# Performance work log

Hardware: AMD Instinct MI355X
Metric: run time of the kernel (lower is better)

Reference implementation:

```python
import jax, jax.numpy as jnp
import numpy as np

D_MODEL = 1024
NHEAD = 16
HEAD_DIM = D_MODEL // NHEAD
D_FF = 4096
LN_EPS = 1e-5


def _layernorm(x, gamma, beta):
    mu = jnp.mean(x, axis=-1, keepdims=True)
    var = jnp.mean(jnp.square(x - mu), axis=-1, keepdims=True)
    return (x - mu) * jax.lax.rsqrt(var + LN_EPS) * gamma + beta


def setup_inputs() -> dict:
    key = jax.random.key(0)
    ks = jax.random.split(key, 16)
    s = 1.0 / np.sqrt(D_MODEL)
    sf = 1.0 / np.sqrt(D_FF)
    inp = {
        "src": jax.random.normal(ks[0], (2, 2048, D_MODEL), dtype=jnp.float32),
        # projection weights stored [in, out]
        "Wq": jax.random.uniform(ks[1], (D_MODEL, D_MODEL), minval=-s, maxval=s),
        "bq": jax.random.uniform(ks[2], (D_MODEL,), minval=-s, maxval=s),
        "Wk": jax.random.uniform(ks[3], (D_MODEL, D_MODEL), minval=-s, maxval=s),
        "bk": jax.random.uniform(ks[4], (D_MODEL,), minval=-s, maxval=s),
        "Wv": jax.random.uniform(ks[5], (D_MODEL, D_MODEL), minval=-s, maxval=s),
        "bv": jax.random.uniform(ks[6], (D_MODEL,), minval=-s, maxval=s),
        "Wo": jax.random.uniform(ks[7], (D_MODEL, D_MODEL), minval=-s, maxval=s),
        "bo": jax.random.uniform(ks[8], (D_MODEL,), minval=-s, maxval=s),
        "W1": jax.random.uniform(ks[9], (D_MODEL, D_FF), minval=-s, maxval=s),
        "b1": jax.random.uniform(ks[10], (D_FF,), minval=-s, maxval=s),
        "W2": jax.random.uniform(ks[11], (D_FF, D_MODEL), minval=-sf, maxval=sf),
        "b2": jax.random.uniform(ks[12], (D_MODEL,), minval=-sf, maxval=sf),
        "gamma1": jnp.ones((D_MODEL,), jnp.float32),
        "beta1": jnp.zeros((D_MODEL,), jnp.float32),
        "gamma2": jnp.ones((D_MODEL,), jnp.float32),
        "beta2": jnp.zeros((D_MODEL,), jnp.float32),
    }
    return inp


def reference(src, Wq, bq, Wk, bk, Wv, bv, Wo, bo, W1, b1, W2, b2,
              gamma1, beta1, gamma2, beta2):
    B, L, D = src.shape
    H, Hd = NHEAD, HEAD_DIM
    # QKV projections -> [B, H, L, Hd]
    def split_heads(x):
        return x.reshape(B, L, H, Hd).transpose(0, 2, 1, 3)
    Q = split_heads(src @ Wq + bq)
    K = split_heads(src @ Wk + bk)
    V = split_heads(src @ Wv + bv)
    # attention (dropout is eval-mode identity)
    scores = jnp.einsum("bhqd,bhkd->bhqk", Q, K) / np.sqrt(Hd)
    probs = jax.nn.softmax(scores, axis=-1)
    attn = jnp.einsum("bhqk,bhkd->bhqd", probs, V)
    attn = attn.transpose(0, 2, 1, 3).reshape(B, L, D)
    attn = attn @ Wo + bo
    x = _layernorm(src + attn, gamma1, beta1)
    ff = jax.nn.gelu(x @ W1 + b1, approximate=False) @ W2 + b2
    return _layernorm(x + ff, gamma2, beta2)
```

## Files before the change

kernel.cpp:

```cpp
#include <hip/hip_runtime.h>
#include <cstdint>
#include <cstddef>

using short8 = short __attribute__((ext_vector_type(8)));
using f32x4  = float __attribute__((ext_vector_type(4)));

__device__ __forceinline__ unsigned short f2bf(float f) {
  unsigned int u = __float_as_uint(f);
  u += 0x7fffu + ((u >> 16) & 1u);
  return (unsigned short)(u >> 16);
}
__device__ __forceinline__ unsigned short f2bf_rhu(float f) {
  return (unsigned short)((__float_as_uint(f) + 0x8000u) >> 16);
}
__device__ __forceinline__ float bf2f(unsigned short s) {
  return __uint_as_float(((unsigned int)s) << 16);
}
__device__ __forceinline__ void async16(const void* g, void* l) {
  __builtin_amdgcn_global_load_lds(
      (const __attribute__((address_space(1))) unsigned int*)g,
      (__attribute__((address_space(3))) unsigned int*)l, 16, 0, 0);
}

#define D_MODEL 1024
#define NHEAD   16
#define HEADD   64
#define SEQL    2048
#define NTOK    4096
#define QSCALE  0.18033688011112042f

__global__ __launch_bounds__(256) void cvt_f32_bf16(const float* __restrict__ in,
                                                    unsigned short* __restrict__ out,
                                                    int n4) {
  int i = blockIdx.x * 256 + threadIdx.x;
  if (i >= n4) return;
  float4 v = ((const float4*)in)[i];
  union { unsigned long long u; unsigned short us[4]; } pk;
  pk.us[0] = f2bf(v.x); pk.us[1] = f2bf(v.y); pk.us[2] = f2bf(v.z); pk.us[3] = f2bf(v.w);
  ((unsigned long long*)out)[i] = pk.u;
}

struct TransTab {
  const float* src[6];
  unsigned short* dst[6];
  int R[6], C[6], start[6], shift[6];
};

__global__ __launch_bounds__(256) void transpose_all(TransTab tt) {
  int id = blockIdx.x, m = 0;
#pragma unroll
  for (int i = 1; i < 6; ++i) if (id >= tt.start[i]) m = i;
  const int local = id - tt.start[m];
  const int R = tt.R[m], C = tt.C[m];
  const int bc = (local & ((1 << tt.shift[m]) - 1)) * 32;
  const int br = (local >> tt.shift[m]) * 32;
  const float* in = tt.src[m];
  unsigned short* out = tt.dst[m];
  __shared__ float tile[32][33];
  const int tx = threadIdx.x & 31, ty = threadIdx.x >> 5;
#pragma unroll
  for (int i = 0; i < 32; i += 8)
    tile[ty + i][tx] = in[(size_t)(br + ty + i) * C + bc + tx];
  __syncthreads();
#pragma unroll
  for (int i = 0; i < 32; i += 8)
    out[(size_t)(bc + ty + i) * R + br + tx] = f2bf(tile[tx][ty + i]);
}

template <int MODE>
__global__ __launch_bounds__(256)
void gemm_bt(const unsigned short* __restrict__ A, const unsigned short* __restrict__ B,
             int M, int N, int K, int Kstride,
             const float* __restrict__ bias0, const float* __restrict__ bias1,
             const float* __restrict__ bias2,
             float* __restrict__ outF, unsigned short* __restrict__ outB,
             unsigned short* __restrict__ outQ, unsigned short* __restrict__ outK,
             unsigned short* __restrict__ outVT) {
  __shared__ __align__(16) short sA[128 * 32];
  __shared__ __align__(16) short sB[128 * 32];
  const int tid = threadIdx.x, wave = tid >> 6, lane = tid & 63;
  const int quad = lane >> 4, l16 = lane & 15;
  const int bm = blockIdx.y * 128, bn = blockIdx.x * 128;
  const int koff = blockIdx.z * K;
  const int wr = (wave >> 1) * 64, wc = (wave & 1) * 64;
  const f32x4 zero4 = {0.f, 0.f, 0.f, 0.f};
  f32x4 acc[4][4];
#pragma unroll
  for (int i = 0; i < 4; ++i)
#pragma unroll
    for (int j = 0; j < 4; ++j) acc[i][j] = zero4;

  for (int kt = 0; kt < K; kt += 32) {
    __syncthreads();
#pragma unroll
    for (int j = 0; j < 2; ++j) {
      int c = (wave * 2 + j) * 64 + lane;
      int row = c >> 2, cp = c & 3;
      int gk = koff + kt + ((cp ^ (row & 3)) * 8);
      async16(A + (size_t)(bm + row) * Kstride + gk, &sA[(wave * 2 + j) * 512]);
      async16(B + (size_t)(bn + row) * Kstride + gk, &sB[(wave * 2 + j) * 512]);
    }
    __syncthreads();
    short8 af[4], bfr[4];
#pragma unroll
    for (int i = 0; i < 4; ++i) {
      int ra = wr + i * 16 + l16;
      af[i] = *(const short8*)&sA[ra * 32 + ((quad ^ (l16 & 3)) * 8)];
      int rb = wc + i * 16 + l16;
      bfr[i] = *(const short8*)&sB[rb * 32 + ((quad ^ (l16 & 3)) * 8)];
    }
#pragma unroll
    for (int mi = 0; mi < 4; ++mi)
#pragma unroll
      for (int ni = 0; ni < 4; ++ni)
        acc[mi][ni] = __builtin_amdgcn_mfma_f32_16x16x32_bf16(af[mi], bfr[ni], acc[mi][ni], 0, 0, 0);
  }

#pragma unroll
  for (int mi = 0; mi < 4; ++mi)
#pragma unroll
    for (int ni = 0; ni < 4; ++ni) {
      const int col = bn + wc + ni * 16 + l16;
      const int row0 = bm + wr + mi * 16 + quad * 4;
      if constexpr (MODE == 0) {
        const int b_ = row0 >> 11, l_ = row0 & 2047;
        if (col < 1024) {
          const int hh = col >> 6, dd = col & 63;
          const size_t o = (((size_t)(b_ * NHEAD + hh)) * SEQL + l_) * HEADD + dd;
#pragma unroll
          for (int r = 0; r < 4; ++r)
            outQ[o + (size_t)r * HEADD] = f2bf((acc[mi][ni][r] + bias0[col]) * QSCALE);
        } else if (col < 2048) {
          const int n2 = col - 1024, hh = n2 >> 6, dd = n2 & 63;
          const size_t o = (((size_t)(b_ * NHEAD + hh)) * SEQL + l_) * HEADD + dd;
#pragma unroll
          for (int r = 0; r < 4; ++r)
            outK[o + (size_t)r * HEADD] = f2bf(acc[mi][ni][r] + bias1[n2]);
        } else {
          const int n2 = col - 2048, hh = n2 >> 6, dd = n2 & 63;
          union { unsigned long long u; unsigned short us[4]; } pk;
#pragma unroll
          for (int r = 0; r < 4; ++r) pk.us[r] = f2bf(acc[mi][ni][r] + bias2[n2]);
          *(unsigned long long*)&outVT[(((size_t)(b_ * NHEAD + hh)) * HEADD + dd) * SEQL + l_] = pk.u;
        }
      } else if constexpr (MODE == 1) {
        float* o = outF + (size_t)blockIdx.z * M * N + (size_t)row0 * N + col;
#pragma unroll
        for (int r = 0; r < 4; ++r) o[(size_t)r * N] = acc[mi][ni][r];
      } else {
#pragma unroll
        for (int r = 0; r < 4; ++r) {
          float x = acc[mi][ni][r] + bias0[col];
          float gl = 0.5f * x * (1.0f + erff(x * 0.70710678118654752f));
          outB[(size_t)(row0 + r) * N + col] = f2bf(gl);
        }
      }
    }
}

__global__ __launch_bounds__(256)
void flash_attn(const unsigned short* __restrict__ Qb, const unsigned short* __restrict__ Kb,
                const unsigned short* __restrict__ VTb, unsigned short* __restrict__ attnA) {
  __shared__ __align__(16) short sK[128 * 64];
  __shared__ __align__(16) short sV[64 * 128];
  __shared__ __align__(16) short sP[128 * 72];
  const int tid = threadIdx.x, wave = tid >> 6, lane = tid & 63;
  const int quad = lane >> 4, l16 = lane & 15;
  const int bh = blockIdx.y;
  const int q0 = blockIdx.x * 128;
  const size_t baseQK = (size_t)bh * SEQL * HEADD;
  const size_t baseV  = (size_t)bh * HEADD * SEQL;

#pragma unroll
  for (int j = 0; j < 4; ++j) {
    int c = (wave * 4 + j) * 64 + lane;
    int row = c >> 3, cp = c & 7;
    int gk = (cp ^ (row & 7)) * 8;
    async16(Qb + baseQK + (size_t)(q0 + row) * HEADD + gk, &sK[(wave * 4 + j) * 512]);
  }
  __syncthreads();
  short8 qf[2][2];
#pragma unroll
  for (int mi = 0; mi < 2; ++mi)
#pragma unroll
    for (int kk = 0; kk < 2; ++kk) {
      int m = wave * 32 + mi * 16 + l16;
      qf[mi][kk] = *(const short8*)&sK[m * 64 + (((kk * 4 + quad) ^ (m & 7)) * 8)];
    }

  const f32x4 zero4 = {0.f, 0.f, 0.f, 0.f};
  f32x4 o_acc[2][4];
  float lsum[2] = {0.f, 0.f};
#pragma unroll
  for (int mi = 0; mi < 2; ++mi)
#pragma unroll
    for (int ni = 0; ni < 4; ++ni) o_acc[mi][ni] = zero4;

  for (int t0 = 0; t0 < SEQL; t0 += 128) {
    __syncthreads();
#pragma unroll
    for (int j = 0; j < 4; ++j) {
      int c = (wave * 4 + j) * 64 + lane;
      { int row = c >> 3, cp = c & 7;
        int gk = (cp ^ (row & 7)) * 8;
        async16(Kb + baseQK + (size_t)(t0 + row) * HEADD + gk, &sK[(wave * 4 + j) * 512]); }
      { int d = c >> 4, cp = c & 15;
        int gl = (cp ^ (d & 15)) * 8;
        async16(VTb + baseV + (size_t)d * SEQL + t0 + gl, &sV[(wave * 4 + j) * 512]); }
    }
    __syncthreads();

#pragma unroll
    for (int h = 0; h < 2; ++h) {
      f32x4 st[4][2];
#pragma unroll
      for (int kt = 0; kt < 4; ++kt)
#pragma unroll
        for (int mi = 0; mi < 2; ++mi) st[kt][mi] = zero4;
#pragma unroll
      for (int kt = 0; kt < 4; ++kt) {
        int krow = (h * 4 + kt) * 16 + l16;
        short8 a0 = *(const short8*)&sK[krow * 64 + ((quad ^ (krow & 7)) * 8)];
        short8 a1 = *(const short8*)&sK[krow * 64 + (((4 + quad) ^ (krow & 7)) * 8)];
#pragma unroll
        for (int mi = 0; mi < 2; ++mi) {
          st[kt][mi] = __builtin_amdgcn_mfma_f32_16x16x32_bf16(a0, qf[mi][0], st[kt][mi], 0, 0, 0);
          st[kt][mi] = __builtin_amdgcn_mfma_f32_16x16x32_bf16(a1, qf[mi][1], st[kt][mi], 0, 0, 0);
        }
      }
#pragma unroll
      for (int kt = 0; kt < 4; ++kt)
#pragma unroll
        for (int mi = 0; mi < 2; ++mi) {
          float e0 = exp2f(st[kt][mi][0]);
          float e1 = exp2f(st[kt][mi][1]);
          float e2 = exp2f(st[kt][mi][2]);
          float e3 = exp2f(st[kt][mi][3]);
          lsum[mi] += (e0 + e1) + (e2 + e3);
          int q = wave * 32 + mi * 16 + l16;
          unsigned int* bp = (unsigned int*)&sP[q * 72 + kt * 16 + quad * 4];
          bp[0] = (unsigned)f2bf_rhu(e0) | ((unsigned)f2bf_rhu(e1) << 16);
          bp[1] = (unsigned)f2bf_rhu(e2) | ((unsigned)f2bf_rhu(e3) << 16);
        }
#pragma unroll
      for (int c = 0; c < 2; ++c) {
        short8 pf[2];
#pragma unroll
        for (int mi = 0; mi < 2; ++mi) {
          int q = wave * 32 + mi * 16 + l16;
          pf[mi] = *(const short8*)&sP[q * 72 + c * 32 + quad * 8];
        }
#pragma unroll
        for (int ni = 0; ni < 4; ++ni) {
          int vrow = ni * 16 + l16;
          short8 vf = *(const short8*)&sV[vrow * 128 + (((h * 8 + c * 4 + quad) ^ (vrow & 15)) * 8)];
#pragma unroll
          for (int mi = 0; mi < 2; ++mi)
            o_acc[mi][ni] = __builtin_amdgcn_mfma_f32_16x16x32_bf16(pf[mi], vf, o_acc[mi][ni], 0, 0, 0);
        }
      }
    }
  }

#pragma unroll
  for (int mi = 0; mi < 2; ++mi) {
    lsum[mi] += __shfl_xor(lsum[mi], 16, 64);
    lsum[mi] += __shfl_xor(lsum[mi], 32, 64);
  }
  const int b_ = bh >> 4, hh = bh & 15;
#pragma unroll
  for (int mi = 0; mi < 2; ++mi)
#pragma unroll
    for (int r = 0; r < 4; ++r) {
      float inv = 1.0f / __shfl(lsum[mi], quad * 4 + r, 64);
      int qrow = q0 + wave * 32 + mi * 16 + quad * 4 + r;
      size_t orow = ((size_t)(b_ * SEQL + qrow)) * D_MODEL + hh * HEADD;
#pragma unroll
      for (int ni = 0; ni < 4; ++ni)
        attnA[orow + ni * 16 + l16] = f2bf(o_acc[mi][ni][r] * inv);
    }
}

__device__ __forceinline__ void ln_core(float x0, float x1, float x2, float x3,
                                        const float* gamma, const float* beta,
                                        int tid, float& y0, float& y1, float& y2, float& y3) {
  float s = x0 + x1 + x2 + x3;
  float q = x0 * x0 + x1 * x1 + x2 * x2 + x3 * x3;
#pragma unroll
  for (int m = 1; m < 64; m <<= 1) {
    s += __shfl_xor(s, m, 64);
    q += __shfl_xor(q, m, 64);
  }
  __shared__ float red[8];
  const int wv = tid >> 6, ln = tid & 63;
  if (ln == 0) { red[wv] = s; red[4 + wv] = q; }
  __syncthreads();
  float S = red[0] + red[1] + red[2] + red[3];
  float Q2 = red[4] + red[5] + red[6] + red[7];
  float mu = S * (1.0f / 1024.0f);
  float var = Q2 * (1.0f / 1024.0f) - mu * mu;
  float rstd = rsqrtf(var + 1e-5f);
  float4 g = ((const float4*)gamma)[tid];
  float4 b = ((const float4*)beta)[tid];
  y0 = (x0 - mu) * rstd * g.x + b.x;
  y1 = (x1 - mu) * rstd * g.y + b.y;
  y2 = (x2 - mu) * rstd * g.z + b.z;
  y3 = (x3 - mu) * rstd * g.w + b.w;
}

__global__ __launch_bounds__(256)
void ln_combine1(const float* __restrict__ p, const float* __restrict__ src,
                 const float* __restrict__ bias, const float* __restrict__ gamma,
                 const float* __restrict__ beta, unsigned short* __restrict__ outB) {
  const int t = blockIdx.x, tid = threadIdx.x;
  const size_t MN = (size_t)NTOK * 1024, base = (size_t)t * 1024;
  float4 a = ((const float4*)(p + base))[tid];
  float4 b4 = ((const float4*)(p + MN + base))[tid];
  float4 s4 = ((const float4*)(src + base))[tid];
  float4 bi = ((const float4*)bias)[tid];
  float y0, y1, y2, y3;
  ln_core(a.x + b4.x + s4.x + bi.x, a.y + b4.y + s4.y + bi.y,
          a.z + b4.z + s4.z + bi.z, a.w + b4.w + s4.w + bi.w,
          gamma, beta, tid, y0, y1, y2, y3);
  union { unsigned long long u; unsigned short us[4]; } pk;
  pk.us[0] = f2bf(y0); pk.us[1] = f2bf(y1); pk.us[2] = f2bf(y2); pk.us[3] = f2bf(y3);
  ((unsigned long long*)(outB + base))[tid] = pk.u;
}

__global__ __launch_bounds__(256)
void ln_combine2(const float* __restrict__ p, const unsigned short* __restrict__ resB,
                 const float* __restrict__ bias, const float* __restrict__ gamma,
                 const float* __restrict__ beta, float* __restrict__ outF) {
  const int t = blockIdx.x, tid = threadIdx.x;
  const size_t MN = (size_t)NTOK * 1024, base = (size_t)t * 1024;
  float4 a = ((const float4*)(p + base))[tid];
  float4 b4 = ((const float4*)(p + MN + base))[tid];
  union { unsigned long long u; unsigned short us[4]; } r;
  r.u = ((const unsigned long long*)(resB + base))[tid];
  float4 bi = ((const float4*)bias)[tid];
  float y0, y1, y2, y3;
  ln_core(a.x + b4.x + bf2f(r.us[0]) + bi.x, a.y + b4.y + bf2f(r.us[1]) + bi.y,
          a.z + b4.z + bf2f(r.us[2]) + bi.z, a.w + b4.w + bf2f(r.us[3]) + bi.w,
          gamma, beta, tid, y0, y1, y2, y3);
  float4 o = {y0, y1, y2, y3};
  ((float4*)(outF + base))[tid] = o;
}

extern "C" void kernel_launch(void* const* d_in, const int* in_sizes, int n_in,
                              void* d_out, int out_size, void* d_ws, size_t ws_size,
                              hipStream_t stream) {
  const float* src    = (const float*)d_in[0];
  const float* Wq     = (const float*)d_in[1];
  const float* bq     = (const float*)d_in[2];
  const float* Wk     = (const float*)d_in[3];
  const float* bk     = (const float*)d_in[4];
  const float* Wv     = (const float*)d_in[5];
  const float* bv     = (const float*)d_in[6];
  const float* Wo     = (const float*)d_in[7];
  const float* bo     = (const float*)d_in[8];
  const float* W1     = (const float*)d_in[9];
  const float* b1     = (const float*)d_in[10];
  const float* W2     = (const float*)d_in[11];
  const float* b2     = (const float*)d_in[12];
  const float* gamma1 = (const float*)d_in[13];
  const float* beta1  = (const float*)d_in[14];
  const float* gamma2 = (const float*)d_in[15];
  const float* beta2  = (const float*)d_in[16];
  float* out = (float*)d_out;
  (void)in_sizes; (void)n_in; (void)out_size; (void)ws_size;

  char* p = (char*)d_ws;
  auto carve = [&](size_t n) { char* r = p; p += (n + 255) & ~(size_t)255; return r; };
  unsigned short* srcB  = (unsigned short*)carve((size_t)NTOK * 1024 * 2);
  unsigned short* WqkvT = (unsigned short*)carve((size_t)3072 * 1024 * 2);
  unsigned short* WoT   = (unsigned short*)carve((size_t)1024 * 1024 * 2);
  unsigned short* W1T   = (unsigned short*)carve((size_t)4096 * 1024 * 2);
  unsigned short* W2T   = (unsigned short*)carve((size_t)1024 * 4096 * 2);
  unsigned short* Qb    = (unsigned short*)carve((size_t)NTOK * 1024 * 2);
  unsigned short* Kb    = (unsigned short*)carve((size_t)NTOK * 1024 * 2);
  unsigned short* VTb   = (unsigned short*)carve((size_t)NTOK * 1024 * 2);
  carve((size_t)NTOK * 1024 * 2);
  unsigned short* xln   = (unsigned short*)carve((size_t)NTOK * 1024 * 2);
  unsigned short* hmid  = (unsigned short*)carve((size_t)NTOK * 4096 * 2);
  unsigned short* attnA = srcB;
  float* partial = (float*)Qb;

  cvt_f32_bf16<<<4096, 256, 0, stream>>>(src, srcB, NTOK * 1024 / 4);
  TransTab tt;
  tt.src[0] = Wq; tt.src[1] = Wk; tt.src[2] = Wv; tt.src[3] = Wo; tt.src[4] = W1; tt.src[5] = W2;
  tt.dst[0] = WqkvT; tt.dst[1] = WqkvT + 1024 * 1024; tt.dst[2] = WqkvT + 2 * 1024 * 1024;
  tt.dst[3] = WoT; tt.dst[4] = W1T; tt.dst[5] = W2T;
  for (int i = 0; i < 4; ++i) { tt.R[i] = 1024; tt.C[i] = 1024; tt.shift[i] = 5; }
  tt.R[4] = 1024; tt.C[4] = 4096; tt.shift[4] = 7;
  tt.R[5] = 4096; tt.C[5] = 1024; tt.shift[5] = 5;
  tt.start[0] = 0; tt.start[1] = 1024; tt.start[2] = 2048; tt.start[3] = 3072;
  tt.start[4] = 4096; tt.start[5] = 8192;
  transpose_all<<<12288, 256, 0, stream>>>(tt);

  gemm_bt<0><<<dim3(24, 32, 1), 256, 0, stream>>>(srcB, WqkvT, NTOK, 3072, 1024, 1024,
                                                  bq, bk, bv, nullptr, nullptr, Qb, Kb, VTb);
  flash_attn<<<dim3(16, 32), 256, 0, stream>>>(Qb, Kb, VTb, attnA);
  gemm_bt<1><<<dim3(8, 32, 2), 256, 0, stream>>>(attnA, WoT, NTOK, 1024, 512, 1024,
                                                 nullptr, nullptr, nullptr, partial,
                                                 nullptr, nullptr, nullptr, nullptr);
  ln_combine1<<<NTOK, 256, 0, stream>>>(partial, src, bo, gamma1, beta1, xln);
  gemm_bt<2><<<dim3(32, 32, 1), 256, 0, stream>>>(xln, W1T, NTOK, 4096, 1024, 1024,
                                                  b1, nullptr, nullptr, nullptr, hmid,
                                                  nullptr, nullptr, nullptr);
  gemm_bt<1><<<dim3(8, 32, 2), 256, 0, stream>>>(hmid, W2T, NTOK, 1024, 2048, 4096,
                                                 nullptr, nullptr, nullptr, partial,
                                                 nullptr, nullptr, nullptr, nullptr);
  ln_combine2<<<NTOK, 256, 0, stream>>>(partial, xln, b2, gamma2, beta2, out);
}
```

Before: 408.5 us.

## Deepen GEMM K tile, add split-K 4, approximate GELU, drop LDS for Q/K

Several independent changes land together. The GEMM now stages 64-wide K tiles with an 8-way XOR swizzle and declares 4 blocks per CU. Split-K for the output projections rises to 4 when workspace allows, and the LN kernels sum a variable number of partials. Exact erf GELU is replaced by a sigmoid-style exp2/rcp approximation. Flash attention reads Q and K fragments straight from global memory instead of staging them in LDS, and uses hardware exp2 plus perm-based bf16 packing. These aim to cut loop and sync overhead and to speed the epilogue math, at the cost of GELU accuracy and more uncoalesced K reads.

```diff
diff --git a/kernel.cpp b/kernel.cpp
--- a/kernel.cpp
+++ b/kernel.cpp
@@ -10,11 +10,13 @@
   u += 0x7fffu + ((u >> 16) & 1u);
   return (unsigned short)(u >> 16);
 }
-__device__ __forceinline__ unsigned short f2bf_rhu(float f) {
-  return (unsigned short)((__float_as_uint(f) + 0x8000u) >> 16);
-}
 __device__ __forceinline__ float bf2f(unsigned short s) {
   return __uint_as_float(((unsigned int)s) << 16);
+}
+__device__ __forceinline__ unsigned int pack_bf16_rhu(float lo, float hi) {
+  unsigned int a = __float_as_uint(lo) + 0x8000u;
+  unsigned int b = __float_as_uint(hi) + 0x8000u;
+  return __builtin_amdgcn_perm(b, a, 0x07060302u);
 }
 __device__ __forceinline__ void async16(const void* g, void* l) {
   __builtin_amdgcn_global_load_lds(
@@ -35,8 +37,9 @@
   int i = blockIdx.x * 256 + threadIdx.x;
   if (i >= n4) return;
   float4 v = ((const float4*)in)[i];
-  union { unsigned long long u; unsigned short us[4]; } pk;
-  pk.us[0] = f2bf(v.x); pk.us[1] = f2bf(v.y); pk.us[2] = f2bf(v.z); pk.us[3] = f2bf(v.w);
+  union { unsigned long long u; unsigned int ui[2]; } pk;
+  pk.ui[0] = pack_bf16_rhu(v.x, v.y);
+  pk.ui[1] = pack_bf16_rhu(v.z, v.w);
   ((unsigned long long*)out)[i] = pk.u;
 }
 
@@ -68,7 +71,7 @@
 }
 
 template <int MODE>
-__global__ __launch_bounds__(256)
+__global__ __launch_bounds__(256, 4)
 void gemm_bt(const unsigned short* __restrict__ A, const unsigned short* __restrict__ B,
              int M, int N, int K, int Kstride,
              const float* __restrict__ bias0, const float* __restrict__ bias1,
@@ -76,8 +79,8 @@
              float* __restrict__ outF, unsigned short* __restrict__ outB,
              unsigned short* __restrict__ outQ, unsigned short* __restrict__ outK,
              unsigned short* __restrict__ outVT) {
-  __shared__ __align__(16) short sA[128 * 32];
-  __shared__ __align__(16) short sB[128 * 32];
+  __shared__ __align__(16) short sA[128 * 64];
+  __shared__ __align__(16) short sB[128 * 64];
   const int tid = threadIdx.x, wave = tid >> 6, lane = tid & 63;
   const int quad = lane >> 4, l16 = lane & 15;
   const int bm = blockIdx.y * 128, bn = blockIdx.x * 128;
@@ -90,30 +93,33 @@
 #pragma unroll
     for (int j = 0; j < 4; ++j) acc[i][j] = zero4;
 
-  for (int kt = 0; kt < K; kt += 32) {
+  for (int kt = 0; kt < K; kt += 64) {
     __syncthreads();
 #pragma unroll
-    for (int j = 0; j < 2; ++j) {
-      int c = (wave * 2 + j) * 64 + lane;
-      int row = c >> 2, cp = c & 3;
-      int gk = koff + kt + ((cp ^ (row & 3)) * 8);
-      async16(A + (size_t)(bm + row) * Kstride + gk, &sA[(wave * 2 + j) * 512]);
-      async16(B + (size_t)(bn + row) * Kstride + gk, &sB[(wave * 2 + j) * 512]);
+    for (int j = 0; j < 4; ++j) {
+      int c = (wave * 4 + j) * 64 + lane;
+      int row = c >> 3, cp = c & 7;
+      int gk = koff + kt + ((cp ^ (row & 7)) * 8);
+      async16(A + (size_t)(bm + row) * Kstride + gk, &sA[(wave * 4 + j) * 512]);
+      async16(B + (size_t)(bn + row) * Kstride + gk, &sB[(wave * 4 + j) * 512]);
     }
     __syncthreads();
-    short8 af[4], bfr[4];
-#pragma unroll
-    for (int i = 0; i < 4; ++i) {
-      int ra = wr + i * 16 + l16;
-      af[i] = *(const short8*)&sA[ra * 32 + ((quad ^ (l16 & 3)) * 8)];
-      int rb = wc + i * 16 + l16;
-      bfr[i] = *(const short8*)&sB[rb * 32 + ((quad ^ (l16 & 3)) * 8)];
-    }
-#pragma unroll
-    for (int mi = 0; mi < 4; ++mi)
-#pragma unroll
-      for (int ni = 0; ni < 4; ++ni)
-        acc[mi][ni] = __builtin_amdgcn_mfma_f32_16x16x32_bf16(af[mi], bfr[ni], acc[mi][ni], 0, 0, 0);
+#pragma unroll
+    for (int kk = 0; kk < 2; ++kk) {
+      short8 af[4], bfr[4];
+#pragma unroll
+      for (int i = 0; i < 4; ++i) {
+        int ra = wr + i * 16 + l16;
+        af[i] = *(const short8*)&sA[ra * 64 + (((kk * 4 + quad) ^ (ra & 7)) * 8)];
+        int rb = wc + i * 16 + l16;
+        bfr[i] = *(const short8*)&sB[rb * 64 + (((kk * 4 + quad) ^ (rb & 7)) * 8)];
+      }
+#pragma unroll
+      for (int mi = 0; mi < 4; ++mi)
+#pragma unroll
+        for (int ni = 0; ni < 4; ++ni)
+          acc[mi][ni] = __builtin_amdgcn_mfma_f32_16x16x32_bf16(af[mi], bfr[ni], acc[mi][ni], 0, 0, 0);
+    }
   }
 
 #pragma unroll
@@ -151,7 +157,10 @@
 #pragma unroll
         for (int r = 0; r < 4; ++r) {
           float x = acc[mi][ni][r] + bias0[col];
-          float gl = 0.5f * x * (1.0f + erff(x * 0.70710678118654752f));
+          float x2 = x * x;
+          float z = x * fmaf(0.102944f, x2, 2.302208f);
+          float t = __builtin_amdgcn_exp2f(z);
+          float gl = x - x * __builtin_amdgcn_rcpf(t + 1.0f);
           outB[(size_t)(row0 + r) * N + col] = f2bf(gl);
         }
       }
@@ -161,7 +170,6 @@
 __global__ __launch_bounds__(256)
 void flash_attn(const unsigned short* __restrict__ Qb, const unsigned short* __restrict__ Kb,
                 const unsigned short* __restrict__ VTb, unsigned short* __restrict__ attnA) {
-  __shared__ __align__(16) short sK[128 * 64];
   __shared__ __align__(16) short sV[64 * 128];
   __shared__ __align__(16) short sP[128 * 72];
   const int tid = threadIdx.x, wave = tid >> 6, lane = tid & 63;
@@ -171,21 +179,13 @@
   const size_t baseQK = (size_t)bh * SEQL * HEADD;
   const size_t baseV  = (size_t)bh * HEADD * SEQL;
 
-#pragma unroll
-  for (int j = 0; j < 4; ++j) {
-    int c = (wave * 4 + j) * 64 + lane;
-    int row = c >> 3, cp = c & 7;
-    int gk = (cp ^ (row & 7)) * 8;
-    async16(Qb + baseQK + (size_t)(q0 + row) * HEADD + gk, &sK[(wave * 4 + j) * 512]);
-  }
-  __syncthreads();
   short8 qf[2][2];
 #pragma unroll
   for (int mi = 0; mi < 2; ++mi)
 #pragma unroll
     for (int kk = 0; kk < 2; ++kk) {
-      int m = wave * 32 + mi * 16 + l16;
-      qf[mi][kk] = *(const short8*)&sK[m * 64 + (((kk * 4 + quad) ^ (m & 7)) * 8)];
+      int q = q0 + wave * 32 + mi * 16 + l16;
+      qf[mi][kk] = *(const short8*)(Qb + baseQK + (size_t)q * HEADD + kk * 32 + quad * 8);
     }
 
   const f32x4 zero4 = {0.f, 0.f, 0.f, 0.f};
@@ -201,12 +201,9 @@
 #pragma unroll
     for (int j = 0; j < 4; ++j) {
       int c = (wave * 4 + j) * 64 + lane;
-      { int row = c >> 3, cp = c & 7;
-        int gk = (cp ^ (row & 7)) * 8;
-        async16(Kb + baseQK + (size_t)(t0 + row) * HEADD + gk, &sK[(wave * 4 + j) * 512]); }
-      { int d = c >> 4, cp = c & 15;
-        int gl = (cp ^ (d & 15)) * 8;
-        async16(VTb + baseV + (size_t)d * SEQL + t0 + gl, &sV[(wave * 4 + j) * 512]); }
+      int d = c >> 4, cp = c & 15;
+      int gl = (cp ^ (d & 15)) * 8;
+      async16(VTb + baseV + (size_t)d * SEQL + t0 + gl, &sV[(wave * 4 + j) * 512]);
     }
     __syncthreads();
 
@@ -219,9 +216,10 @@
         for (int mi = 0; mi < 2; ++mi) st[kt][mi] = zero4;
 #pragma unroll
       for (int kt = 0; kt < 4; ++kt) {
-        int krow = (h * 4 + kt) * 16 + l16;
-        short8 a0 = *(const short8*)&sK[krow * 64 + ((quad ^ (krow & 7)) * 8)];
-        short8 a1 = *(const short8*)&sK[krow * 64 + (((4 + quad) ^ (krow & 7)) * 8)];
+        const unsigned short* kp =
+            Kb + baseQK + (size_t)(t0 + h * 64 + kt * 16 + l16) * HEADD + quad * 8;
+        short8 a0 = *(const short8*)(kp);
+        short8 a1 = *(const short8*)(kp + 32);
 #pragma unroll
         for (int mi = 0; mi < 2; ++mi) {
           st[kt][mi] = __builtin_amdgcn_mfma_f32_16x16x32_bf16(a0, qf[mi][0], st[kt][mi], 0, 0, 0);
@@ -232,15 +230,16 @@
       for (int kt = 0; kt < 4; ++kt)
 #pragma unroll
         for (int mi = 0; mi < 2; ++mi) {
-          float e0 = exp2f(st[kt][mi][0]);
-          float e1 = exp2f(st[kt][mi][1]);
-          float e2 = exp2f(st[kt][mi][2]);
-          float e3 = exp2f(st[kt][mi][3]);
+          float e0 = __builtin_amdgcn_exp2f(st[kt][mi][0]);
+          float e1 = __builtin_amdgcn_exp2f(st[kt][mi][1]);
+          float e2 = __builtin_amdgcn_exp2f(st[kt][mi][2]);
+          float e3 = __builtin_amdgcn_exp2f(st[kt][mi][3]);
           lsum[mi] += (e0 + e1) + (e2 + e3);
           int q = wave * 32 + mi * 16 + l16;
-          unsigned int* bp = (unsigned int*)&sP[q * 72 + kt * 16 + quad * 4];
-          bp[0] = (unsigned)f2bf_rhu(e0) | ((unsigned)f2bf_rhu(e1) << 16);
-          bp[1] = (unsigned)f2bf_rhu(e2) | ((unsigned)f2bf_rhu(e3) << 16);
+          union { unsigned long long u; unsigned int ui[2]; } pk;
+          pk.ui[0] = pack_bf16_rhu(e0, e1);
+          pk.ui[1] = pack_bf16_rhu(e2, e3);
+          *(unsigned long long*)&sP[q * 72 + kt * 16 + quad * 4] = pk.u;
         }
 #pragma unroll
       for (int c = 0; c < 2; ++c) {
@@ -309,38 +308,45 @@
 }
 
 __global__ __launch_bounds__(256)
-void ln_combine1(const float* __restrict__ p, const float* __restrict__ src,
+void ln_combine1(const float* __restrict__ p, int nsplit, const float* __restrict__ src,
                  const float* __restrict__ bias, const float* __restrict__ gamma,
                  const float* __restrict__ beta, unsigned short* __restrict__ outB) {
   const int t = blockIdx.x, tid = threadIdx.x;
   const size_t MN = (size_t)NTOK * 1024, base = (size_t)t * 1024;
   float4 a = ((const float4*)(p + base))[tid];
-  float4 b4 = ((const float4*)(p + MN + base))[tid];
+  for (int s = 1; s < nsplit; ++s) {
+    float4 b4 = ((const float4*)(p + s * MN + base))[tid];
+    a.x += b4.x; a.y += b4.y; a.z += b4.z; a.w += b4.w;
+  }
   float4 s4 = ((const float4*)(src + base))[tid];
   float4 bi = ((const float4*)bias)[tid];
   float y0, y1, y2, y3;
-  ln_core(a.x + b4.x + s4.x + bi.x, a.y + b4.y + s4.y + bi.y,
-          a.z + b4.z + s4.z + bi.z, a.w + b4.w + s4.w + bi.w,
+  ln_core(a.x + s4.x + bi.x, a.y + s4.y + bi.y,
+          a.z + s4.z + bi.z, a.w + s4.w + bi.w,
           gamma, beta, tid, y0, y1, y2, y3);
-  union { unsigned long long u; unsigned short us[4]; } pk;
-  pk.us[0] = f2bf(y0); pk.us[1] = f2bf(y1); pk.us[2] = f2bf(y2); pk.us[3] = f2bf(y3);
+  union { unsigned long long u; unsigned int ui[2]; } pk;
+  pk.ui[0] = (unsigned)f2bf(y0) | ((unsigned)f2bf(y1) << 16);
+  pk.ui[1] = (unsigned)f2bf(y2) | ((unsigned)f2bf(y3) << 16);
   ((unsigned long long*)(outB + base))[tid] = pk.u;
 }
 
 __global__ __launch_bounds__(256)
-void ln_combine2(const float* __restrict__ p, const unsigned short* __restrict__ resB,
+void ln_combine2(const float* __restrict__ p, int nsplit, const unsigned short* __restrict__ resB,
                  const float* __restrict__ bias, const float* __restrict__ gamma,
                  const float* __restrict__ beta, float* __restrict__ outF) {
   const int t = blockIdx.x, tid = threadIdx.x;
   const size_t MN = (size_t)NTOK * 1024, base = (size_t)t * 1024;
   float4 a = ((const float4*)(p + base))[tid];
-  float4 b4 = ((const float4*)(p + MN + base))[tid];
+  for (int s = 1; s < nsplit; ++s) {
+    float4 b4 = ((const float4*)(p + s * MN + base))[tid];
+    a.x += b4.x; a.y += b4.y; a.z += b4.z; a.w += b4.w;
+  }
   union { unsigned long long u; unsigned short us[4]; } r;
   r.u = ((const unsigned long long*)(resB + base))[tid];
   float4 bi = ((const float4*)bias)[tid];
   float y0, y1, y2, y3;
-  ln_core(a.x + b4.x + bf2f(r.us[0]) + bi.x, a.y + b4.y + bf2f(r.us[1]) + bi.y,
-          a.z + b4.z + bf2f(r.us[2]) + bi.z, a.w + b4.w + bf2f(r.us[3]) + bi.w,
+  ln_core(a.x + bf2f(r.us[0]) + bi.x, a.y + bf2f(r.us[1]) + bi.y,
+          a.z + bf2f(r.us[2]) + bi.z, a.w + bf2f(r.us[3]) + bi.w,
           gamma, beta, tid, y0, y1, y2, y3);
   float4 o = {y0, y1, y2, y3};
   ((float4*)(outF + base))[tid] = o;
@@ -367,10 +373,13 @@
   const float* gamma2 = (const float*)d_in[15];
   const float* beta2  = (const float*)d_in[16];
   float* out = (float*)d_out;
-  (void)in_sizes; (void)n_in; (void)out_size; (void)ws_size;
+  (void)in_sizes; (void)n_in; (void)out_size;
 
   char* p = (char*)d_ws;
-  auto carve = [&](size_t n) { char* r = p; p += (n + 255) & ~(size_t)255; return r; };
+  size_t used = 0;
+  auto carve = [&](size_t n) {
+    char* r = p; size_t a = (n + 255) & ~(size_t)255; p += a; used += a; return r;
+  };
   unsigned short* srcB  = (unsigned short*)carve((size_t)NTOK * 1024 * 2);
   unsigned short* WqkvT = (unsigned short*)carve((size_t)3072 * 1024 * 2);
   unsigned short* WoT   = (unsigned short*)carve((size_t)1024 * 1024 * 2);
@@ -383,7 +392,11 @@
   unsigned short* xln   = (unsigned short*)carve((size_t)NTOK * 1024 * 2);
   unsigned short* hmid  = (unsigned short*)carve((size_t)NTOK * 4096 * 2);
   unsigned short* attnA = srcB;
-  float* partial = (float*)Qb;
+  float* partial2 = (float*)Qb;
+  const size_t need4 = (size_t)NTOK * 1024 * 4 * 4;
+  float* partial4 = (ws_size >= used + need4) ? (float*)carve(need4) : nullptr;
+  const int nsplit = partial4 ? 4 : 2;
+  float* partial = partial4 ? partial4 : partial2;
 
   cvt_f32_bf16<<<4096, 256, 0, stream>>>(src, srcB, NTOK * 1024 / 4);
   TransTab tt;
@@ -400,15 +413,15 @@
   gemm_bt<0><<<dim3(24, 32, 1), 256, 0, stream>>>(srcB, WqkvT, NTOK, 3072, 1024, 1024,
                                                   bq, bk, bv, nullptr, nullptr, Qb, Kb, VTb);
   flash_attn<<<dim3(16, 32), 256, 0, stream>>>(Qb, Kb, VTb, attnA);
-  gemm_bt<1><<<dim3(8, 32, 2), 256, 0, stream>>>(attnA, WoT, NTOK, 1024, 512, 1024,
-                                                 nullptr, nullptr, nullptr, partial,
-                                                 nullptr, nullptr, nullptr, nullptr);
-  ln_combine1<<<NTOK, 256, 0, stream>>>(partial, src, bo, gamma1, beta1, xln);
+  gemm_bt<1><<<dim3(8, 32, nsplit), 256, 0, stream>>>(attnA, WoT, NTOK, 1024, 1024 / nsplit, 1024,
+                                                      nullptr, nullptr, nullptr, partial,
+                                                      nullptr, nullptr, nullptr, nullptr);
+  ln_combine1<<<NTOK, 256, 0, stream>>>(partial, nsplit, src, bo, gamma1, beta1, xln);
   gemm_bt<2><<<dim3(32, 32, 1), 256, 0, stream>>>(xln, W1T, NTOK, 4096, 1024, 1024,
                                                   b1, nullptr, nullptr, nullptr, hmid,
                                                   nullptr, nullptr, nullptr);
-  gemm_bt<1><<<dim3(8, 32, 2), 256, 0, stream>>>(hmid, W2T, NTOK, 1024, 2048, 4096,
-                                                 nullptr, nullptr, nullptr, partial,
-                                                 nullptr, nullptr, nullptr, nullptr);
-  ln_combine2<<<NTOK, 256, 0, stream>>>(partial, xln, b2, gamma2, beta2, out);
-}
+  gemm_bt<1><<<dim3(8, 32, nsplit), 256, 0, stream>>>(hmid, W2T, NTOK, 1024, 4096 / nsplit, 4096,
+                                                      nullptr, nullptr, nullptr, partial,
+                                                      nullptr, nullptr, nullptr, nullptr);
+  ln_combine2<<<NTOK, 256, 0, stream>>>(partial, nsplit, xln, b2, gamma2, beta2, out);
+}
```

Measured after the change: 391.9 us. 1.04x faster.
